# Performance work log

Hardware: AMD Instinct MI355X
Metric: run time of the kernel (lower is better)

Reference implementation:

```python
import jax, jax.numpy as jnp
import numpy as np

B, S = 64, 100
N_EX, N_Q = 3000, 128
N_AT, N_IT = 1000, 1000
D_A = D_E = D_K = 128
GAMMA = 0.03


def _xavier(k, shape):
    lim = float(np.sqrt(6.0 / (shape[0] + shape[1])))
    return jax.random.uniform(k, shape, jnp.float32, -lim, lim)


def setup_inputs() -> dict:
    key = jax.random.key(0)
    ks = jax.random.split(key, 20)
    nq1 = N_Q + 1
    e_data = jax.random.randint(ks[0], (B, S), 0, N_EX, dtype=jnp.int32)
    a_data = jax.random.randint(ks[1], (B, S), 0, 2, dtype=jnp.int32)
    it_data = jax.random.randint(ks[2], (B, S), 0, N_IT, dtype=jnp.int32)
    at_data = jax.random.randint(ks[3], (B, S), 0, N_AT, dtype=jnp.int32)
    # binary Q-matrix with zeros replaced by gamma (as done in LPKT.__init__)
    q_bin = (jax.random.uniform(ks[4], (N_EX + 10, nq1)) < 0.05).astype(jnp.float32)
    q_matrix = jnp.where(q_bin > 0, 1.0, GAMMA)
    E_at = _xavier(ks[5], (N_AT + 10, D_K))
    E_it = _xavier(ks[6], (N_IT + 10, D_K))
    E_e = _xavier(ks[7], (N_EX + 10, D_E))
    h0 = _xavier(ks[8], (nq1, D_K))  # xavier-initialized initial skill state
    W1 = _xavier(ks[9], (D_A + D_E + D_K, D_K)); b1 = jnp.zeros(D_K, jnp.float32)
    W2 = _xavier(ks[10], (4 * D_K, D_K)); b2 = jnp.zeros(D_K, jnp.float32)
    W3 = _xavier(ks[11], (4 * D_K, D_K)); b3 = jnp.zeros(D_K, jnp.float32)
    W4 = _xavier(ks[12], (3 * D_K, D_K)); b4 = jnp.zeros(D_K, jnp.float32)
    W5 = _xavier(ks[13], (D_E + D_K, D_K)); b5 = jnp.zeros(D_K, jnp.float32)
    return dict(e_data=e_data, a_data=a_data, it_data=it_data, at_data=at_data,
                q_matrix=q_matrix, h0=h0, E_e=E_e, E_at=E_at, E_it=E_it,
                W1=W1, b1=b1, W2=W2, b2=b2, W3=W3, b3=b3, W4=W4, b4=b4, W5=W5, b5=b5)


def reference(e_data, a_data, it_data, at_data, q_matrix, h0, E_e, E_at, E_it,
              W1, b1, W2, b2, W3, b3, W4, b4, W5, b5):
    Bv, Sv = e_data.shape
    d_k = W2.shape[1]
    d_a = W1.shape[0] - E_e.shape[1] - d_k
    e_emb = E_e[e_data]            # (B,S,d_e)
    at_emb = E_at[at_data]         # (B,S,d_k)
    it_emb = E_it[it_data]         # (B,S,d_k)
    a_rep = jnp.broadcast_to(a_data.astype(jnp.float32)[..., None], (Bv, Sv, d_a))
    all_learning = jnp.concatenate([e_emb, at_emb, a_rep], 2) @ W1 + b1  # (B,S,d_k)
    q_all = q_matrix[e_data]       # (B,S,nq1)
    h_pre0 = jnp.broadcast_to(h0, (Bv,) + h0.shape)  # (B,nq1,d_k)
    q0 = q_all[:, 0]
    ht0 = jnp.einsum('bn,bnd->bd', q0, h_pre0) / q0.sum(1, keepdims=True)
    W4h, W4l, W4i = jnp.split(W4, 3, axis=0)

    def step(carry, x):
        learning_pre, h_pre, h_tilde_pre = carry
        q_e, q_next, it, learning, e_next = x
        feat = jnp.concatenate([learning_pre, it, learning, h_tilde_pre], 1)  # (B,4dk)
        lg = jnp.tanh(feat @ W2 + b2)
        gamma_l = jax.nn.sigmoid(feat @ W3 + b3)
        LG = gamma_l * (lg + 1.0) * 0.5                       # (B,d_k)
        LG_tilde = q_e[:, :, None] * LG[:, None, :]           # (B,nq1,d_k); dropout=eval identity
        gamma_f = jax.nn.sigmoid(jnp.einsum('bnd,df->bnf', h_pre, W4h)
                                 + (LG @ W4l + it @ W4i + b4)[:, None, :])
        h = LG_tilde + gamma_f * h_pre
        h_tilde = jnp.einsum('bn,bnd->bd', q_next, h) / q_next.sum(1, keepdims=True)
        y = jax.nn.sigmoid(jnp.concatenate([e_next, h_tilde], 1) @ W5 + b5).sum(1) / d_k
        return (learning, h, h_tilde), y

    xs = (jnp.swapaxes(q_all[:, :-1], 0, 1), jnp.swapaxes(q_all[:, 1:], 0, 1),
          jnp.swapaxes(it_emb[:, :-1], 0, 1), jnp.swapaxes(all_learning[:, :-1], 0, 1),
          jnp.swapaxes(e_emb[:, 1:], 0, 1))
    learning_pre0 = jnp.zeros((Bv, d_k), jnp.float32)
    _, ys = jax.lax.scan(step, (learning_pre0, h_pre0, ht0), xs)  # ys: (S-1,B)
    pred = jnp.zeros((Bv, Sv), jnp.float32).at[:, 1:].set(ys.T)
    return pred
```

## Files before the change

kernel.cpp:

```cpp
#include <hip/hip_runtime.h>
#include <hip/hip_fp16.h>
#include <math.h>


#define BB   64
#define SS   100
#define DK   128
#define NTH  512

#define OFF_PW1AB   0
#define OFF_PW23ABC 16384
#define OFF_PW4I    65536
#define OFF_PW5A    73728
#define OFF_PW23D   81920
#define OFF_PW4L    98304
#define OFF_AFRAG   114688
#define OFF_S1      122880
#define OFF_AL      123008
#define OFF_PRE     532608
#define OFF_HTV     2171008

typedef __attribute__((ext_vector_type(16))) float floatx16;
typedef __attribute__((ext_vector_type(8)))  short short8v;
typedef __attribute__((ext_vector_type(2)))  float floatx2;

__device__ __forceinline__ float frcp(float x) { return __builtin_amdgcn_rcpf(x); }
__device__ __forceinline__ float fsig(float x) { float t = __expf(-x); return frcp(1.0f + t); }
__device__ __forceinline__ float ftanh(float x) {
    x = fminf(20.0f, fmaxf(-20.0f, x));
    float t = __expf(-2.0f * x);
    return (1.0f - t) * frcp(1.0f + t);
}
__device__ __forceinline__ unsigned bfbits(float x) {
    unsigned u = __float_as_uint(x);
    return (u + 0x7fffu + ((u >> 16) & 1u)) >> 16;
}
__device__ __forceinline__ unsigned pack2(float a, float b) {
    return bfbits(a) | (bfbits(b) << 16);
}
__device__ __forceinline__ float blo(unsigned u) { return __uint_as_float(u << 16); }
__device__ __forceinline__ float bhi(unsigned u) { return __uint_as_float(u & 0xffff0000u); }

__device__ __forceinline__ unsigned cvtpk(float a, float b) {
    unsigned r;
    asm("v_cvt_pk_bf16_f32 %0, %1, %2" : "=v"(r) : "v"(a), "v"(b));
    return r;
}

__device__ __forceinline__ void wg_barrier() {
    asm volatile("s_waitcnt lgkmcnt(0)" ::: "memory");
    __builtin_amdgcn_s_barrier();
    asm volatile("" ::: "memory");
}

__global__ void k0_prep(const float* __restrict__ W1, const float* __restrict__ W2,
                        const float* __restrict__ W3, const float* __restrict__ W4,
                        const float* __restrict__ W5, unsigned* __restrict__ ws) {
    int g = blockIdx.x * blockDim.x + threadIdx.x;
    if (g < 16384) {
        int s = g >> 7, d = g & 127;
        ws[OFF_PW1AB + g] = pack2(W1[(2*s)*DK + d], W1[(2*s+1)*DK + d]);
    } else if (g < 65536) {
        int i = g - 16384; int s = i >> 8, j = i & 255;
        const float* M = (j < 128) ? W2 : W3; int jj = j & 127;
        ws[g] = pack2(M[(2*s)*DK + jj], M[(2*s+1)*DK + jj]);
    } else if (g < 73728) {
        int i = g - 65536; int s = i >> 7, j = i & 127;
        ws[g] = pack2(W4[(256+2*s)*DK + j], W4[(257+2*s)*DK + j]);
    } else if (g < 81920) {
        int i = g - 73728; int s = i >> 7, j = i & 127;
        ws[g] = pack2(W5[(2*s)*DK + j], W5[(2*s+1)*DK + j]);
    } else if (g < 98304) {
        int i = g - 81920;
        int q = i & 3, ln = (i >> 2) & 63, kb = (i >> 8) & 7, cw = i >> 11;
        int k = 16*kb + 8*(ln >> 5) + 2*q;
        int j = 32*cw + (ln & 31);
        const float* M = (j < 128) ? W2 : W3; int jj = j & 127;
        ws[g] = pack2(M[(384+k)*DK + jj], M[(385+k)*DK + jj]);
    } else if (g < 106496) {
        int i = g - 98304;
        int q = i & 3, ln = (i >> 2) & 63, kb = (i >> 8) & 7, cw = i >> 11;
        int k = 16*kb + 8*(ln >> 5) + 2*q;
        int j = 32*cw + (ln & 31);
        ws[g] = pack2(W4[(128+k)*DK + j], W4[(129+k)*DK + j]);
    } else if (g < 114688) {
    } else if (g < 122880) {
        int i = g - 114688;
        int gg = i >> 11, kb = (i >> 8) & 7, ln = (i >> 2) & 63, c = i & 3;
        int m = ln & 31, hp = ln >> 5;
        int k0 = 16*kb + 8*hp + 2*c;
        ws[g] = pack2(W4[k0*DK + 32*gg + m], W4[(k0+1)*DK + 32*gg + m]);
    } else if (g < 123008) {
        int d = g - 122880;
        float z = 0.f;
        for (int k = 0; k < 128; k++) z += W1[(256+k)*DK + d];
        ws[g] = __float_as_uint(z);
    }
}

__global__ __launch_bounds__(128)
void k1_al(const int* __restrict__ e_data, const int* __restrict__ a_data,
           const int* __restrict__ at_data, const float* __restrict__ Ee,
           const float* __restrict__ Eat, const float* __restrict__ b1,
           unsigned* __restrict__ ws) {
    const int b = blockIdx.x, t0 = 8 * blockIdx.y, tid = threadIdx.x;
    __shared__ __align__(16) float s_f[8][256];
    #pragma unroll
    for (int r = 0; r < 16; r++) {
        int id = r * 128 + tid; int i = id >> 8, k = id & 255;
        int t = t0 + i; float v = 0.f;
        if (t <= 98) {
            int e  = e_data[b*SS + t];
            int at = at_data[b*SS + t];
            v = (k < 128) ? Ee[(size_t)e*DK + k] : Eat[(size_t)at*DK + (k-128)];
        }
        s_f[i][k] = v;
    }
    __syncthreads();
    float s1v = __uint_as_float(ws[OFF_S1 + tid]);
    float b1v = b1[tid];
    float z[8];
    #pragma unroll
    for (int i = 0; i < 8; i++) z[i] = 0.f;
    #pragma unroll 2
    for (int s = 0; s < 128; s++) {
        unsigned w = ws[OFF_PW1AB + s*128 + tid];
        float wl = blo(w), wh = bhi(w);
        #pragma unroll
        for (int i = 0; i < 8; i++) {
            float2 f = *(const float2*)&s_f[i][2*s];
            z[i] += f.x*wl + f.y*wh;
        }
    }
    __half* AL = (__half*)(ws + OFF_AL);
    #pragma unroll
    for (int i = 0; i < 8; i++) {
        int t = t0 + i;
        if (t <= 98) {
            float a = (float)a_data[b*SS + t];
            AL[(size_t)(b*SS + t)*DK + tid] = __float2half(z[i] + a*s1v + b1v);
        }
    }
}

__global__ __launch_bounds__(512)
void k2_pre(const int* __restrict__ e_data, const int* __restrict__ it_data,
            const float* __restrict__ Eit, const float* __restrict__ Ee,
            const float* __restrict__ b2, const float* __restrict__ b3,
            const float* __restrict__ b4, const float* __restrict__ b5,
            unsigned* __restrict__ ws) {
    const int b = blockIdx.x, t0 = 8 * blockIdx.y, tid = threadIdx.x;
    __shared__ __align__(16) float s_g[8][384];
    __shared__ __align__(16) float s_e[8][128];
    const __half* AL = (const __half*)(ws + OFF_AL);
    #pragma unroll
    for (int r = 0; r < 6; r++) {
        int id = r * 512 + tid; int i = id / 384; int k = id - 384*i;
        int t = t0 + i; float v = 0.f;
        if (t <= 98) {
            if (k < 128)      v = (t == 0) ? 0.f : (float)AL[(size_t)(b*SS + t - 1)*DK + k];
            else if (k < 256) v = Eit[(size_t)it_data[b*SS + t]*DK + (k - 128)];
            else              v = (float)AL[(size_t)(b*SS + t)*DK + (k - 256)];
        }
        s_g[i][k] = v;
    }
    #pragma unroll
    for (int r = 0; r < 2; r++) {
        int id = r * 512 + tid; int i = id >> 7, k = id & 127;
        int t = t0 + i;
        s_e[i][k] = (t <= 98) ? Ee[(size_t)e_data[b*SS + t + 1]*DK + k] : 0.f;
    }
    __syncthreads();
    __half* PRE = (__half*)(ws + OFF_PRE);
    float z[8];
    #pragma unroll
    for (int i = 0; i < 8; i++) z[i] = 0.f;
    int col; float bb;
    if (tid < 256) {
        int j = tid;
        #pragma unroll 2
        for (int s = 0; s < 192; s++) {
            unsigned w = ws[OFF_PW23ABC + s*256 + j];
            float wl = blo(w), wh = bhi(w);
            #pragma unroll
            for (int i = 0; i < 8; i++) {
                float2 f = *(const float2*)&s_g[i][2*s];
                z[i] += f.x*wl + f.y*wh;
            }
        }
        col = j; bb = (j < 128) ? b2[j] : b3[j - 128];
    } else if (tid < 384) {
        int j = tid - 256;
        #pragma unroll 2
        for (int s = 0; s < 64; s++) {
            unsigned w = ws[OFF_PW4I + s*128 + j];
            float wl = blo(w), wh = bhi(w);
            #pragma unroll
            for (int i = 0; i < 8; i++) {
                float2 f = *(const float2*)&s_g[i][128 + 2*s];
                z[i] += f.x*wl + f.y*wh;
            }
        }
        col = 256 + j; bb = b4[j];
    } else {
        int j = tid - 384;
        #pragma unroll 2
        for (int s = 0; s < 64; s++) {
            unsigned w = ws[OFF_PW5A + s*128 + j];
            float wl = blo(w), wh = bhi(w);
            #pragma unroll
            for (int i = 0; i < 8; i++) {
                float2 f = *(const float2*)&s_e[i][2*s];
                z[i] += f.x*wl + f.y*wh;
            }
        }
        col = 384 + j; bb = b5[j];
    }
    #pragma unroll
    for (int i = 0; i < 8; i++) {
        int t = t0 + i;
        if (t <= 98) PRE[(size_t)(b*SS + t)*512 + col] = __float2half(z[i] + bb);
    }
}

__global__ __launch_bounds__(NTH, 2)
void lpkt_kernel(const int* __restrict__ e_data, const float* __restrict__ qm,
                 const float* __restrict__ h0, unsigned* __restrict__ ws)
{
    const int b    = blockIdx.x;
    const int tid  = threadIdx.x;
    const int lane = tid & 63;
    const int w    = tid >> 6;
    const int g    = w & 3;
    const int hh   = w >> 2;
    const int h5   = lane >> 5;
    const int l31  = lane & 31;
    const int hf   = w >> 2;
    const int cw3  = w & 3;

    __shared__ __align__(16) unsigned s_frag[8192];
    __shared__ __align__(16) float s_big[2 * 128 * 34];
    __shared__ __align__(16) float s_pre[2][512];
    __shared__ __align__(16) float s_LG[128];
    __shared__ __align__(16) float s_h128[128];
    __shared__ __align__(16) float s_l128[2][128];
    __shared__ __align__(16) float s_red1[256];
    __shared__ __align__(16) float s_redE[256];
    __shared__ __align__(16) unsigned s_htvb[64];
    __shared__ __align__(16) float s_q[3][160];
    __shared__ int   s_ed[100];
    __shared__ float s_scal[2];

    uint4    afru[8], pw23b[8], pw4lb[4];
    floatx2  hreg2[2][8];
    floatx16 am[2];

    #pragma unroll
    for (int kb = 0; kb < 8; kb++)
        afru[kb] = ((const uint4*)(ws + OFF_AFRAG))[g*512 + kb*64 + lane];
    #pragma unroll
    for (int kb = 0; kb < 8; kb++)
        pw23b[kb] = ((const uint4*)(ws + OFF_PW23D))[(w*8 + kb)*64 + lane];
    #pragma unroll
    for (int kbl = 0; kbl < 4; kbl++)
        pw4lb[kbl] = ((const uint4*)(ws + OFF_PW4L))[((cw3*8 + hf*4 + kbl))*64 + lane];

    const __half* PRE = (const __half*)(ws + OFF_PRE);
    __half*       HTV = (__half*)(ws + OFF_HTV);

    if (tid < 100) s_ed[tid] = e_data[b*SS + tid];
    if (tid < 160) { s_q[0][tid] = 0.f; s_q[1][tid] = 0.f; s_q[2][tid] = 0.f; }
    if (tid < 129) {
        s_q[0][tid] = qm[(size_t)e_data[b*SS + 0]*129 + tid];
        s_q[1][tid] = qm[(size_t)e_data[b*SS + 1]*129 + tid];
    }
    s_pre[0][tid] = __half2float(PRE[(size_t)(b*SS)*512 + tid]);
    float  q_pf   = (tid < 129) ? qm[(size_t)e_data[b*SS + 2]*129 + tid] : 0.f;
    __half pre_pf = PRE[(size_t)(b*SS + 1)*512 + tid];

    #pragma unroll
    for (int i = 0; i < 2; i++) {
        const int cb = 2*hh + i;
        const int n = 32*cb + l31;
        #pragma unroll
        for (int m = 0; m < 8; m++) {
            int r = 2*m;
            int d = 32*g + (r&3) + 8*(r>>2) + 4*h5;
            hreg2[i][m] = *(const floatx2*)&h0[(size_t)n*DK + d];
        }
        #pragma unroll
        for (int q = 0; q < 4; q++) {
            int kb = 2*g + (q>>1);
            int lanep = l31 + ((q&1) << 5);
            int off = (((kb*4 + cb) << 10) + lanep*16 + (h5 << 3)) >> 2;
            uint2 pr = make_uint2(cvtpk(hreg2[i][2*q].x,   hreg2[i][2*q].y),
                                  cvtpk(hreg2[i][2*q+1].x, hreg2[i][2*q+1].y));
            *(uint2*)(s_frag + off) = pr;
        }
    }
    if (tid < 128) s_h128[tid] = h0[(size_t)128*DK + tid];
    __syncthreads();

    {
        if (w == 7) {
            float v0 = s_q[0][lane] + s_q[0][64+lane] + ((lane < 32) ? s_q[0][128+lane] : 0.f);
            float v1 = s_q[1][lane] + s_q[1][64+lane] + ((lane < 32) ? s_q[1][128+lane] : 0.f);
            #pragma unroll
            for (int m = 32; m > 0; m >>= 1) { v0 += __shfl_xor(v0, m); v1 += __shfl_xor(v1, m); }
            if (lane == 0) { s_scal[0] = v0; s_scal[1] = v1; }
        }
        floatx2 vv0[8];
        #pragma unroll
        for (int i = 0; i < 2; i++) {
            float qv = s_q[0][32*(2*hh + i) + l31];
            floatx2 qv2 = {qv, qv};
            #pragma unroll
            for (int m = 0; m < 8; m++) {
                if (i == 0) vv0[m] = qv2 * hreg2[i][m];
                else        vv0[m] = vv0[m] + qv2 * hreg2[i][m];
            }
        }
        #pragma unroll
        for (int m = 0; m < 8; m++) {
            int r = 2*m;
            int d = 32*g + (r&3) + 8*(r>>2) + 4*h5;
            s_big[(hh*128 + d)*34 + l31]       = vv0[m].x;
            s_big[(hh*128 + d + 1)*34 + l31]   = vv0[m].y;
        }
        #pragma unroll
        for (int i = 0; i < 2; i++) {
            const int cb = 2*hh + i;
            floatx16 a = (floatx16)(0.f);
            #pragma unroll
            for (int kb = 0; kb < 8; kb++) {
                short8v bf = *(const short8v*)((const char*)s_frag +
                               (((kb*4 + cb) << 10) + lane*16));
                a = __builtin_amdgcn_mfma_f32_32x32x16_bf16(
                        __builtin_bit_cast(short8v, afru[kb]), bf, a, 0, 0, 0);
            }
            am[i] = a;
        }
    }
    __syncthreads();

    {
        const int row = 16*w + (lane >> 2);
        const int qr  = lane & 3;
        const float* basep = &s_big[(((qr >> 1) << 7) + row)*34 + ((qr & 1) << 4)];
        floatx2 a2 = {0.f, 0.f};
        #pragma unroll
        for (int jj = 0; jj < 8; jj++)
            a2 = a2 + *(const floatx2*)(basep + 2*jj);
        float a0 = a2.x + a2.y;
        a0 += __shfl_xor(a0, 1);
        a0 += __shfl_xor(a0, 2);
        float htvv = (a0 + s_q[0][128]*s_h128[row]) * frcp(s_scal[0]);
        float oth = __shfl_down(htvv, 4);
        if ((lane & 7) == 0) s_htvb[row >> 1] = cvtpk(htvv, oth);
    }
    __syncthreads();

    for (int t = 0; t < SS - 1; t++) {
        const int pbp = t & 1;
        const float* qc = s_q[t % 3];
        const float* qn = s_q[(t + 1) % 3];

        if (t + 2 <= 99 && tid < 129) s_q[(t + 2) % 3][tid] = q_pf;
        if (t + 1 <= 98)              s_pre[1 - pbp][tid] = __half2float(pre_pf);
        if (t + 3 <= 99 && tid < 129) q_pf  = qm[(size_t)s_ed[t + 3]*129 + tid];
        if (t + 2 <= 98)              pre_pf = PRE[(size_t)(b*SS + t + 2)*512 + tid];
        {
            floatx16 p1 = (floatx16)(0.f);
            #pragma unroll
            for (int kb = 0; kb < 8; kb++) {
                uint4 a1 = *(const uint4*)&s_htvb[kb*8 + 4*h5];
                p1 = __builtin_amdgcn_mfma_f32_32x32x16_bf16(
                        __builtin_bit_cast(short8v, a1),
                        __builtin_bit_cast(short8v, pw23b[kb]), p1, 0, 0, 0);
            }
            if (h5 == 0) s_red1[w*32 + l31] = p1[0];
        }
        wg_barrier();
        {
            const int m = 64*hf + lane;
            float z2v = s_red1[m]       + s_pre[pbp][m];
            float z3v = s_red1[128 + m] + s_pre[pbp][128 + m];
            float LGv = fsig(z3v) * (ftanh(z2v) + 1.f) * 0.5f;
            if (cw3 == 0) s_LG[m] = LGv;
            float oth = __shfl_xor(LGv, 1);
            float lo  = (lane & 1) ? oth : LGv;
            float hi  = (lane & 1) ? LGv : oth;
            int   pk  = (int)cvtpk(lo, hi);
            floatx16 p3 = (floatx16)(0.f);
            #pragma unroll
            for (int kbl = 0; kbl < 4; kbl++) {
                const int p0 = 8*kbl + 4*h5;
                uint4 a3;
                a3.x = (unsigned)__builtin_amdgcn_ds_bpermute(8*(p0+0), pk);
                a3.y = (unsigned)__builtin_amdgcn_ds_bpermute(8*(p0+1), pk);
                a3.z = (unsigned)__builtin_amdgcn_ds_bpermute(8*(p0+2), pk);
                a3.w = (unsigned)__builtin_amdgcn_ds_bpermute(8*(p0+3), pk);
                p3 = __builtin_amdgcn_mfma_f32_32x32x16_bf16(
                        __builtin_bit_cast(short8v, a3),
                        __builtin_bit_cast(short8v, pw4lb[kbl]), p3, 0, 0, 0);
            }
            if (h5 == 0) s_redE[hf*128 + 32*cw3 + l31] = p3[0];
        }
        wg_barrier();
        {
            floatx2 lg2[8], cv2[8], vv2[8];
            const float4* LG4 = (const float4*)s_LG;
            const float4* RE4 = (const float4*)s_redE;
            const float4* PR4 = (const float4*)s_pre[pbp];
            #pragma unroll
            for (int u = 0; u < 4; u++) {
                const int idx = 8*g + 2*u + h5;
                float4 lg = LG4[idx];
                float4 c0 = RE4[idx];
                float4 c1 = RE4[32 + idx];
                float4 pv = PR4[64 + idx];
                lg2[2*u]   = floatx2{lg.x, lg.y};
                lg2[2*u+1] = floatx2{lg.z, lg.w};
                cv2[2*u]   = floatx2{c0.x, c0.y} + floatx2{c1.x, c1.y} + floatx2{pv.x, pv.y};
                cv2[2*u+1] = floatx2{c0.z, c0.w} + floatx2{c1.z, c1.w} + floatx2{pv.z, pv.w};
            }
            const floatx2 nl2e2 = {-1.442695041f, -1.442695041f};
            #pragma unroll
            for (int i = 0; i < 2; i++) {
                const int cb = 2*hh + i;
                const int n = 32*cb + l31;
                const float qcv = qc[n], qnv = qn[n];
                const floatx2 qc2 = {qcv, qcv};
                const floatx2 qn2 = {qnv, qnv};
                #pragma unroll
                for (int m = 0; m < 8; m++) {
                    floatx2 x2 = floatx2{am[i][2*m], am[i][2*m+1]} + cv2[m];
                    floatx2 t2 = x2 * nl2e2;
                    floatx2 e2 = {__builtin_amdgcn_exp2f(t2.x), __builtin_amdgcn_exp2f(t2.y)};
                    floatx2 g2 = {frcp(1.f + e2.x), frcp(1.f + e2.y)};
                    floatx2 hn2 = qc2 * lg2[m] + g2 * hreg2[i][m];
                    hreg2[i][m] = hn2;
                    if (i == 0) vv2[m] = qn2 * hn2;
                    else        vv2[m] = vv2[m] + qn2 * hn2;
                }
            }
            #pragma unroll
            for (int i = 0; i < 2; i++) {
                const int cb = 2*hh + i;
                #pragma unroll
                for (int q = 0; q < 4; q++) {
                    int kb = 2*g + (q>>1);
                    int lanep = l31 + ((q&1) << 5);
                    int off = (((kb*4 + cb) << 10) + lanep*16 + (h5 << 3)) >> 2;
                    uint2 pr = make_uint2(cvtpk(hreg2[i][2*q].x,   hreg2[i][2*q].y),
                                          cvtpk(hreg2[i][2*q+1].x, hreg2[i][2*q+1].y));
                    *(uint2*)(s_frag + off) = pr;
                }
            }
            #pragma unroll
            for (int m = 0; m < 8; m++) {
                int r = 2*m;
                int d = 32*g + (r&3) + 8*(r>>2) + 4*h5;
                s_big[(hh*128 + d)*34 + l31]     = vv2[m].x;
                s_big[(hh*128 + d + 1)*34 + l31] = vv2[m].y;
            }
            if (tid < 128) {
                float c128 = s_redE[tid] + s_redE[128 + tid] + s_pre[pbp][256 + tid];
                float gg = fsig(s_l128[0][tid] + s_l128[1][tid] + c128);
                s_h128[tid] = qc[128]*s_LG[tid] + gg*s_h128[tid];
            }
        }
        wg_barrier();
        #pragma unroll
        for (int i = 0; i < 2; i++) {
            const int cb = 2*hh + i;
            floatx16 a = (floatx16)(0.f);
            #pragma unroll
            for (int kb = 0; kb < 8; kb++) {
                short8v bf = *(const short8v*)((const char*)s_frag +
                               (((kb*4 + cb) << 10) + lane*16));
                a = __builtin_amdgcn_mfma_f32_32x32x16_bf16(
                        __builtin_bit_cast(short8v, afru[kb]), bf, a, 0, 0, 0);
            }
            am[i] = a;
        }
        {
            float part = 0.f;
            #pragma unroll
            for (int kbl = 0; kbl < 4; kbl++) {
                const int kb = 4*hh + kbl;
                const int kb0 = 16*kb + 8*h5;
                uint4 u = afru[kb];
                part += s_h128[kb0+0]*blo(u.x) + s_h128[kb0+1]*bhi(u.x);
                part += s_h128[kb0+2]*blo(u.y) + s_h128[kb0+3]*bhi(u.y);
                part += s_h128[kb0+4]*blo(u.z) + s_h128[kb0+5]*bhi(u.z);
                part += s_h128[kb0+6]*blo(u.w) + s_h128[kb0+7]*bhi(u.w);
            }
            part += __shfl_xor(part, 32);
            if (h5 == 0) s_l128[hh][32*g + l31] = part;
        }
        if (w == 7 && t + 2 <= 99) {
            const float* q2 = s_q[(t + 2) % 3];
            float v = q2[lane] + q2[64 + lane] + ((lane < 32) ? q2[128 + lane] : 0.f);
            #pragma unroll
            for (int m = 32; m > 0; m >>= 1) v += __shfl_xor(v, m);
            if (lane == 0) s_scal[(t + 2) & 1] = v;
        }
        {
            const int row = 16*w + (lane >> 2);
            const int qr  = lane & 3;
            const float* basep = &s_big[(((qr >> 1) << 7) + row)*34 + ((qr & 1) << 4)];
            floatx2 a2 = {0.f, 0.f};
            #pragma unroll
            for (int jj = 0; jj < 8; jj++)
                a2 = a2 + *(const floatx2*)(basep + 2*jj);
            float a0 = a2.x + a2.y;
            a0 += __shfl_xor(a0, 1);
            a0 += __shfl_xor(a0, 2);
            float htvv = (a0 + qn[128]*s_h128[row]) * frcp(s_scal[(t + 1) & 1]);
            if (qr == 0)
                HTV[((size_t)b*(SS-1) + t)*128 + row] = __float2half(htvv);
            float oth = __shfl_down(htvv, 4);
            if ((lane & 7) == 0) s_htvb[row >> 1] = cvtpk(htvv, oth);
        }
        wg_barrier();
    }
}

__global__ __launch_bounds__(128)
void k4_y(const float* __restrict__ W5, float* __restrict__ out,
          const unsigned* __restrict__ ws) {
    const int b = blockIdx.x, t = blockIdx.y, j = threadIdx.x;
    const __half* HTV = (const __half*)(ws + OFF_HTV);
    const __half* PRE = (const __half*)(ws + OFF_PRE);
    __shared__ float s_h[128];
    __shared__ float s_p[2];
    s_h[j] = __half2float(HTV[((size_t)b*(SS-1) + t)*128 + j]);
    __syncthreads();
    float z = __half2float(PRE[(size_t)(b*SS + t)*512 + 384 + j]);
    #pragma unroll 4
    for (int k = 0; k < 128; k++) z += s_h[k] * W5[(size_t)(128 + k)*DK + j];
    float v = fsig(z);
    #pragma unroll
    for (int m = 32; m > 0; m >>= 1) v += __shfl_xor(v, m);
    if ((j & 63) == 0) s_p[j >> 6] = v;
    __syncthreads();
    if (j == 0) {
        out[b*SS + t + 1] = (s_p[0] + s_p[1]) * (1.0f / 128.0f);
        if (t == 0) out[b*SS] = 0.f;
    }
}

extern "C" void kernel_launch(void* const* d_in, const int* in_sizes, int n_in,
                              void* d_out, int out_size, void* d_ws, size_t ws_size,
                              hipStream_t stream) {
    const int*   e_data  = (const int*)d_in[0];
    const int*   a_data  = (const int*)d_in[1];
    const int*   it_data = (const int*)d_in[2];
    const int*   at_data = (const int*)d_in[3];
    const float* qm  = (const float*)d_in[4];
    const float* h0  = (const float*)d_in[5];
    const float* Ee  = (const float*)d_in[6];
    const float* Eat = (const float*)d_in[7];
    const float* Eit = (const float*)d_in[8];
    const float* W1  = (const float*)d_in[9];
    const float* b1  = (const float*)d_in[10];
    const float* W2  = (const float*)d_in[11];
    const float* b2  = (const float*)d_in[12];
    const float* W3  = (const float*)d_in[13];
    const float* b3  = (const float*)d_in[14];
    const float* W4  = (const float*)d_in[15];
    const float* b4  = (const float*)d_in[16];
    const float* W5  = (const float*)d_in[17];
    const float* b5  = (const float*)d_in[18];
    float* out = (float*)d_out;
    unsigned* ws = (unsigned*)d_ws;

    k0_prep<<<dim3((123008 + 255) / 256), dim3(256), 0, stream>>>(W1, W2, W3, W4, W5, ws);
    k1_al<<<dim3(BB, 13), dim3(128), 0, stream>>>(e_data, a_data, at_data, Ee, Eat, b1, ws);
    k2_pre<<<dim3(BB, 13), dim3(512), 0, stream>>>(e_data, it_data, Eit, Ee, b2, b3, b4, b5, ws);
    lpkt_kernel<<<dim3(BB), dim3(NTH), 0, stream>>>(e_data, qm, h0, ws);
    k4_y<<<dim3(BB, SS - 1), dim3(128), 0, stream>>>(W5, out, ws);
}
```

Baseline: 657.6 us.

## Fuse learning-embedding kernel into pre-projection kernel and batch output kernel over timesteps

Merges the all_learning (W1) computation into the pre-projection kernel. Each block recomputes its 9 needed learning rows (including the previous timestep) into shared memory instead of writing them to and reading them back from a half-precision workspace. This removes one launch and the global round trip, at the cost of recomputing one overlapping row per block. The output kernel now processes 8 timesteps per block, reusing each W5 load across 8 rows and cutting the grid from 64x99 to 64x13 blocks. Precision changes slightly because the learning vectors are no longer rounded to half before use.

```diff
diff --git a/kernel.cpp b/kernel.cpp
--- a/kernel.cpp
+++ b/kernel.cpp
@@ -98,77 +98,70 @@
     }
 }
 
-__global__ __launch_bounds__(128)
-void k1_al(const int* __restrict__ e_data, const int* __restrict__ a_data,
-           const int* __restrict__ at_data, const float* __restrict__ Ee,
-           const float* __restrict__ Eat, const float* __restrict__ b1,
-           unsigned* __restrict__ ws) {
+__global__ __launch_bounds__(512)
+void k2_pre(const int* __restrict__ e_data, const int* __restrict__ a_data,
+            const int* __restrict__ at_data, const int* __restrict__ it_data,
+            const float* __restrict__ Ee, const float* __restrict__ Eat,
+            const float* __restrict__ Eit,
+            const float* __restrict__ b1, const float* __restrict__ b2,
+            const float* __restrict__ b3, const float* __restrict__ b4,
+            const float* __restrict__ b5, unsigned* __restrict__ ws) {
     const int b = blockIdx.x, t0 = 8 * blockIdx.y, tid = threadIdx.x;
-    __shared__ __align__(16) float s_f[8][256];
-    #pragma unroll
-    for (int r = 0; r < 16; r++) {
-        int id = r * 128 + tid; int i = id >> 8, k = id & 255;
-        int t = t0 + i; float v = 0.f;
-        if (t <= 98) {
-            int e  = e_data[b*SS + t];
-            int at = at_data[b*SS + t];
-            v = (k < 128) ? Ee[(size_t)e*DK + k] : Eat[(size_t)at*DK + (k-128)];
-        }
-        s_f[i][k] = v;
-    }
-    __syncthreads();
-    float s1v = __uint_as_float(ws[OFF_S1 + tid]);
-    float b1v = b1[tid];
-    float z[8];
-    #pragma unroll
-    for (int i = 0; i < 8; i++) z[i] = 0.f;
-    #pragma unroll 2
-    for (int s = 0; s < 128; s++) {
-        unsigned w = ws[OFF_PW1AB + s*128 + tid];
-        float wl = blo(w), wh = bhi(w);
-        #pragma unroll
-        for (int i = 0; i < 8; i++) {
-            float2 f = *(const float2*)&s_f[i][2*s];
-            z[i] += f.x*wl + f.y*wh;
-        }
-    }
-    __half* AL = (__half*)(ws + OFF_AL);
-    #pragma unroll
-    for (int i = 0; i < 8; i++) {
-        int t = t0 + i;
-        if (t <= 98) {
-            float a = (float)a_data[b*SS + t];
-            AL[(size_t)(b*SS + t)*DK + tid] = __float2half(z[i] + a*s1v + b1v);
-        }
-    }
-}
-
-__global__ __launch_bounds__(512)
-void k2_pre(const int* __restrict__ e_data, const int* __restrict__ it_data,
-            const float* __restrict__ Eit, const float* __restrict__ Ee,
-            const float* __restrict__ b2, const float* __restrict__ b3,
-            const float* __restrict__ b4, const float* __restrict__ b5,
-            unsigned* __restrict__ ws) {
-    const int b = blockIdx.x, t0 = 8 * blockIdx.y, tid = threadIdx.x;
-    __shared__ __align__(16) float s_g[8][384];
+    __shared__ __align__(16) float s_f[9][256];
+    __shared__ __align__(16) float s_al[9][128];
+    __shared__ __align__(16) float s_it[8][128];
     __shared__ __align__(16) float s_e[8][128];
-    const __half* AL = (const __half*)(ws + OFF_AL);
-    #pragma unroll
-    for (int r = 0; r < 6; r++) {
-        int id = r * 512 + tid; int i = id / 384; int k = id - 384*i;
-        int t = t0 + i; float v = 0.f;
-        if (t <= 98) {
-            if (k < 128)      v = (t == 0) ? 0.f : (float)AL[(size_t)(b*SS + t - 1)*DK + k];
-            else if (k < 256) v = Eit[(size_t)it_data[b*SS + t]*DK + (k - 128)];
-            else              v = (float)AL[(size_t)(b*SS + t)*DK + (k - 256)];
-        }
-        s_g[i][k] = v;
+    #pragma unroll
+    for (int r = 0; r < 5; r++) {
+        int id = r * 512 + tid;
+        if (id < 2304) {
+            int i = id >> 8, k = id & 255;
+            int t = t0 - 1 + i; float v = 0.f;
+            if (t >= 0 && t <= 98) {
+                int e  = e_data[b*SS + t];
+                int at = at_data[b*SS + t];
+                v = (k < 128) ? Ee[(size_t)e*DK + k] : Eat[(size_t)at*DK + (k-128)];
+            }
+            s_f[i][k] = v;
+        }
     }
     #pragma unroll
     for (int r = 0; r < 2; r++) {
         int id = r * 512 + tid; int i = id >> 7, k = id & 127;
         int t = t0 + i;
-        s_e[i][k] = (t <= 98) ? Ee[(size_t)e_data[b*SS + t + 1]*DK + k] : 0.f;
+        s_it[i][k] = (t <= 98) ? Eit[(size_t)it_data[b*SS + t]*DK + k] : 0.f;
+        s_e[i][k]  = (t <= 98) ? Ee[(size_t)e_data[b*SS + t + 1]*DK + k] : 0.f;
+    }
+    __syncthreads();
+    {
+        const int d = tid & 127, p = tid >> 7;
+        const int nt = (p == 0) ? 3 : 2;
+        int   tl[3]; tl[0] = p; tl[1] = p + 4; tl[2] = p + 8;
+        float zal[3] = {0.f, 0.f, 0.f};
+        float s1v = __uint_as_float(ws[OFF_S1 + d]);
+        float b1v = b1[d];
+        #pragma unroll 2
+        for (int s = 0; s < 128; s++) {
+            unsigned w = ws[OFF_PW1AB + s*128 + d];
+            float wl = blo(w), wh = bhi(w);
+            #pragma unroll
+            for (int q = 0; q < 3; q++) {
+                if (q < nt) {
+                    float2 f = *(const float2*)&s_f[tl[q]][2*s];
+                    zal[q] += f.x*wl + f.y*wh;
+                }
+            }
+        }
+        #pragma unroll
+        for (int q = 0; q < 3; q++) {
+            if (q < nt) {
+                int i = tl[q], t = t0 - 1 + i;
+                float v = 0.f;
+                if (t >= 0 && t <= 98)
+                    v = zal[q] + (float)a_data[b*SS + t]*s1v + b1v;
+                s_al[i][d] = v;
+            }
+        }
     }
     __syncthreads();
     __half* PRE = (__half*)(ws + OFF_PRE);
@@ -179,12 +172,32 @@
     if (tid < 256) {
         int j = tid;
         #pragma unroll 2
-        for (int s = 0; s < 192; s++) {
+        for (int s = 0; s < 64; s++) {
             unsigned w = ws[OFF_PW23ABC + s*256 + j];
             float wl = blo(w), wh = bhi(w);
             #pragma unroll
             for (int i = 0; i < 8; i++) {
-                float2 f = *(const float2*)&s_g[i][2*s];
+                float2 f = *(const float2*)&s_al[i][2*s];
+                z[i] += f.x*wl + f.y*wh;
+            }
+        }
+        #pragma unroll 2
+        for (int s = 64; s < 128; s++) {
+            unsigned w = ws[OFF_PW23ABC + s*256 + j];
+            float wl = blo(w), wh = bhi(w);
+            #pragma unroll
+            for (int i = 0; i < 8; i++) {
+                float2 f = *(const float2*)&s_it[i][2*(s-64)];
+                z[i] += f.x*wl + f.y*wh;
+            }
+        }
+        #pragma unroll 2
+        for (int s = 128; s < 192; s++) {
+            unsigned w = ws[OFF_PW23ABC + s*256 + j];
+            float wl = blo(w), wh = bhi(w);
+            #pragma unroll
+            for (int i = 0; i < 8; i++) {
+                float2 f = *(const float2*)&s_al[i+1][2*(s-128)];
                 z[i] += f.x*wl + f.y*wh;
             }
         }
@@ -197,7 +210,7 @@
             float wl = blo(w), wh = bhi(w);
             #pragma unroll
             for (int i = 0; i < 8; i++) {
-                float2 f = *(const float2*)&s_g[i][128 + 2*s];
+                float2 f = *(const float2*)&s_it[i][2*s];
                 z[i] += f.x*wl + f.y*wh;
             }
         }
@@ -530,25 +543,42 @@
 __global__ __launch_bounds__(128)
 void k4_y(const float* __restrict__ W5, float* __restrict__ out,
           const unsigned* __restrict__ ws) {
-    const int b = blockIdx.x, t = blockIdx.y, j = threadIdx.x;
+    const int b = blockIdx.x, t0 = 8 * blockIdx.y, j = threadIdx.x;
     const __half* HTV = (const __half*)(ws + OFF_HTV);
     const __half* PRE = (const __half*)(ws + OFF_PRE);
-    __shared__ float s_h[128];
-    __shared__ float s_p[2];
-    s_h[j] = __half2float(HTV[((size_t)b*(SS-1) + t)*128 + j]);
+    __shared__ __align__(16) float s_h[8][128];
+    __shared__ float s_p[8][2];
+    #pragma unroll
+    for (int i = 0; i < 8; i++) {
+        int t = t0 + i;
+        s_h[i][j] = (t <= 98) ? __half2float(HTV[((size_t)b*(SS-1) + t)*128 + j]) : 0.f;
+    }
     __syncthreads();
-    float z = __half2float(PRE[(size_t)(b*SS + t)*512 + 384 + j]);
-    #pragma unroll 4
-    for (int k = 0; k < 128; k++) z += s_h[k] * W5[(size_t)(128 + k)*DK + j];
-    float v = fsig(z);
-    #pragma unroll
-    for (int m = 32; m > 0; m >>= 1) v += __shfl_xor(v, m);
-    if ((j & 63) == 0) s_p[j >> 6] = v;
+    float z[8];
+    #pragma unroll
+    for (int i = 0; i < 8; i++) {
+        int t = t0 + i;
+        z[i] = (t <= 98) ? __half2float(PRE[(size_t)(b*SS + t)*512 + 384 + j]) : 0.f;
+    }
+    #pragma unroll 2
+    for (int k = 0; k < 128; k++) {
+        float w = W5[(size_t)(128 + k)*DK + j];
+        #pragma unroll
+        for (int i = 0; i < 8; i++) z[i] += s_h[i][k] * w;
+    }
+    #pragma unroll
+    for (int i = 0; i < 8; i++) {
+        float v = fsig(z[i]);
+        #pragma unroll
+        for (int m = 32; m > 0; m >>= 1) v += __shfl_xor(v, m);
+        if ((j & 63) == 0) s_p[i][j >> 6] = v;
+    }
     __syncthreads();
-    if (j == 0) {
-        out[b*SS + t + 1] = (s_p[0] + s_p[1]) * (1.0f / 128.0f);
-        if (t == 0) out[b*SS] = 0.f;
-    }
+    if (j < 8) {
+        int t = t0 + j;
+        if (t <= 98) out[b*SS + t + 1] = (s_p[j][0] + s_p[j][1]) * (1.0f / 128.0f);
+    }
+    if (j == 8 && t0 == 0) out[b*SS] = 0.f;
 }
 
 extern "C" void kernel_launch(void* const* d_in, const int* in_sizes, int n_in,
@@ -577,8 +607,8 @@
     unsigned* ws = (unsigned*)d_ws;
 
     k0_prep<<<dim3((123008 + 255) / 256), dim3(256), 0, stream>>>(W1, W2, W3, W4, W5, ws);
-    k1_al<<<dim3(BB, 13), dim3(128), 0, stream>>>(e_data, a_data, at_data, Ee, Eat, b1, ws);
-    k2_pre<<<dim3(BB, 13), dim3(512), 0, stream>>>(e_data, it_data, Eit, Ee, b2, b3, b4, b5, ws);
+    k2_pre<<<dim3(BB, 13), dim3(512), 0, stream>>>(e_data, a_data, at_data, it_data,
+                                                   Ee, Eat, Eit, b1, b2, b3, b4, b5, ws);
     lpkt_kernel<<<dim3(BB), dim3(NTH), 0, stream>>>(e_data, qm, h0, ws);
-    k4_y<<<dim3(BB, SS - 1), dim3(128), 0, stream>>>(W5, out, ws);
-}
+    k4_y<<<dim3(BB, 13), dim3(128), 0, stream>>>(W5, out, ws);
+}
```

After: 668.2 us. No clear change (+1.6%).
